# Kernel tuning notes

Hardware: AMD Instinct MI355X
Metric: run time of the kernel (lower is better)

Reference implementation:

```python
import jax, jax.numpy as jnp
import numpy as np

K_STEPS = 2  # number of staged propagation levels encoded in edge_mask


def _propagate(h, src, dst, mask, num_nodes):
    """KPropagate: K staged scatter-add steps over the edge list.

    Step k sums messages along edges with edge_mask == k; later steps
    propagate the freshly aggregated values (rule-node fan-out).
    """
    out = jnp.zeros_like(h)
    cur = h
    for k in range(K_STEPS):
        msg = jnp.where((mask == k)[:, None], cur[src], jnp.zeros((), h.dtype))  # [E, F]
        out = out + jax.ops.segment_sum(msg, dst, num_segments=num_nodes)
        cur = out
    return out


def setup_inputs() -> dict:
    key = jax.random.key(0)
    ks = jax.random.split(key, 8)
    V, R = 50000, 10000
    N = V + R
    E = 160000
    F_IN, F_OUT = 512, 128
    x = jax.random.normal(ks[0], (N, F_IN), dtype=jnp.float32)
    edge_index = jax.random.randint(ks[1], (2, E), 0, N, dtype=jnp.int64)
    edge_mask = jax.random.randint(ks[2], (E,), 0, K_STEPS, dtype=jnp.int64)
    # lin1: in_features -> in_features; lin2: in_features -> out_features
    s1 = 1.0 / np.sqrt(F_IN)
    W1 = jax.random.uniform(ks[3], (F_IN, F_IN), jnp.float32, -s1, s1)
    b1 = jax.random.uniform(ks[4], (F_IN,), jnp.float32, -s1, s1)
    W2 = jax.random.uniform(ks[5], (F_IN, F_OUT), jnp.float32, -s1, s1)
    b2 = jax.random.uniform(ks[6], (F_OUT,), jnp.float32, -s1, s1)
    return {"x": x, "edge_index": edge_index, "edge_mask": edge_mask,
            "vertex_cnt": V, "rule_cnt": R,
            "W1": W1, "b1": b1, "W2": W2, "b2": b2}


def reference(x, edge_index, edge_mask, vertex_cnt, rule_cnt, W1, b1, W2, b2):
    N = x.shape[0]  # == vertex_cnt + rule_cnt
    src, dst = edge_index[0], edge_index[1]
    h = x @ W1 + b1                                   # lin1
    h = jax.nn.relu(_propagate(h, src, dst, edge_mask, N))  # P1 -> relu
    h = h @ W2 + b2                                   # lin2
    h = _propagate(h, src, dst, edge_mask, N)         # P2
    # NOTE: original code computes log_softmax into `out` but returns x (=h).
    return h
```

## Files before the change

### kernel.cpp

```cpp
#include <hip/hip_runtime.h>

typedef __bf16 bf16x8 __attribute__((ext_vector_type(8)));
typedef float  floatx4 __attribute__((ext_vector_type(4)));
typedef unsigned short ushortx8 __attribute__((ext_vector_type(8)));
typedef unsigned short ushortx4 __attribute__((ext_vector_type(4)));
typedef unsigned short ushortx2 __attribute__((ext_vector_type(2)));

__device__ __forceinline__ float bf2f(unsigned short u) {
    return __uint_as_float(((unsigned)u) << 16);
}
__device__ __forceinline__ unsigned short f2bf(float f) {
    unsigned u = __float_as_uint(f);
    return (unsigned short)((u + 0x7FFFu + ((u >> 16) & 1u)) >> 16);
}

__device__ __forceinline__ void gload_lds16(const unsigned short* g, unsigned short* l) {
    __builtin_amdgcn_global_load_lds(
        (const __attribute__((address_space(1))) void*)g,
        (__attribute__((address_space(3))) void*)l, 16, 0, 0);
}

__global__ void cvt_f32_bf16_kernel(const float* __restrict__ in,
                                    unsigned short* __restrict__ out, int n4) {
    int i = blockIdx.x * blockDim.x + threadIdx.x;
    if (i >= n4) return;
    float4 v = ((const float4*)in)[i];
    ushortx4 o;
    o[0] = f2bf(v.x); o[1] = f2bf(v.y); o[2] = f2bf(v.z); o[3] = f2bf(v.w);
    ((ushortx4*)out)[i] = o;
}

__global__ void transpose_cvt_kernel(const float* __restrict__ in,
                                     unsigned short* __restrict__ out,
                                     int K, int N) {
    int idx = blockIdx.x * blockDim.x + threadIdx.x;
    if (idx >= K * N) return;
    int k = idx / N, n = idx - k * N;
    out[n * K + k] = f2bf(in[idx]);
}

__global__ void init_head_kernel(int* __restrict__ head, int n) {
    int i = blockIdx.x * blockDim.x + threadIdx.x;
    if (i < n) head[i] = -1;
}

__global__ void build_list_kernel(const int* __restrict__ ei, int E,
                                  int* __restrict__ head, int* __restrict__ nxt) {
    int e = blockIdx.x * blockDim.x + threadIdx.x;
    if (e >= E) return;
    int d = ei[E + e];
    nxt[e] = atomicExch(&head[d], e);
}

#define BM 128
#define BN 128
#define BK 32

__global__ __launch_bounds__(256) void gemm_bt_bias(
    const unsigned short* __restrict__ A,
    const unsigned short* __restrict__ Bt,
    const float* __restrict__ bias,
    unsigned short* __restrict__ C,
    int M, int N, int K)
{
    __shared__ unsigned short Sh[8192];
    unsigned short (*As)[512] = (unsigned short(*)[512])Sh;
    unsigned short (*Bs)[512] = (unsigned short(*)[512])(Sh + 4096);

    const int tid  = threadIdx.x;
    const int lane = tid & 63;
    const int wave = tid >> 6;
    const int bM = blockIdx.y * BM;
    const int bN = blockIdx.x * BN;
    const int wm = (wave >> 1) * 64;
    const int wn = (wave & 1) * 64;
    const int q    = lane >> 4;
    const int mrow = lane & 15;

    int rA0 = bM + wave * 16 + mrow;        if (rA0 >= M) rA0 = M - 1;
    int rA1 = bM + (wave + 4) * 16 + mrow;  if (rA1 >= M) rA1 = M - 1;
    const int rB0 = bN + wave * 16 + mrow;
    const int rB1 = bN + (wave + 4) * 16 + mrow;
    const unsigned short* gA0 = A  + (size_t)rA0 * K + q * 8;
    const unsigned short* gA1 = A  + (size_t)rA1 * K + q * 8;
    const unsigned short* gB0 = Bt + (size_t)rB0 * K + q * 8;
    const unsigned short* gB1 = Bt + (size_t)rB1 * K + q * 8;

    floatx4 acc[4][4];
#pragma unroll
    for (int i = 0; i < 4; i++)
#pragma unroll
        for (int j = 0; j < 4; j++) acc[i][j] = (floatx4)(0.0f);

    for (int kt = 0; kt < K; kt += BK) {
        gload_lds16(gA0 + kt, &As[wave][0]);
        gload_lds16(gA1 + kt, &As[wave + 4][0]);
        gload_lds16(gB0 + kt, &Bs[wave][0]);
        gload_lds16(gB1 + kt, &Bs[wave + 4][0]);
        __syncthreads();

        bf16x8 af[4], bfv[4];
#pragma unroll
        for (int mi = 0; mi < 4; mi++)
            af[mi] = *(const bf16x8*)&As[(wave >> 1) * 4 + mi][lane * 8];
#pragma unroll
        for (int ni = 0; ni < 4; ni++)
            bfv[ni] = *(const bf16x8*)&Bs[(wave & 1) * 4 + ni][lane * 8];
#pragma unroll
        for (int mi = 0; mi < 4; mi++)
#pragma unroll
            for (int ni = 0; ni < 4; ni++)
                acc[mi][ni] = __builtin_amdgcn_mfma_f32_16x16x32_bf16(
                    af[mi], bfv[ni], acc[mi][ni], 0, 0, 0);
        __syncthreads();
    }

    unsigned short* lbuf = Sh + wave * 2048;
    float bv[4];
#pragma unroll
    for (int ni = 0; ni < 4; ni++) bv[ni] = bias[bN + wn + ni * 16 + mrow];

#pragma unroll
    for (int p = 0; p < 2; p++) {
#pragma unroll
        for (int mh = 0; mh < 2; mh++) {
            int mi = 2 * p + mh;
#pragma unroll
            for (int ni = 0; ni < 4; ni++)
#pragma unroll
                for (int r = 0; r < 4; r++)
                    lbuf[(mh * 16 + q * 4 + r) * 64 + ni * 16 + mrow] =
                        f2bf(acc[mi][ni][r] + bv[ni]);
        }
#pragma unroll
        for (int i = 0; i < 4; i++) {
            int prow = i * 8 + (lane >> 3);
            int pcol = (lane & 7) * 8;
            int grow = bM + wm + p * 32 + prow;
            if (grow < M)
                *(ushortx8*)(C + (size_t)grow * N + bN + wn + pcol) =
                    *(const ushortx8*)&lbuf[prow * 64 + pcol];
        }
    }
}

template <int VEC> struct VecT;
template <> struct VecT<8> { typedef ushortx8 type; };
template <> struct VecT<2> { typedef ushortx2 type; };

template <int VEC, bool ADD_SELF, bool RELU, bool OUT_F32>
__global__ __launch_bounds__(256) void prop_step_kernel(
    const unsigned short* __restrict__ cur,
    void* __restrict__ outp,
    const int* __restrict__ head,
    const int* __restrict__ nxt,
    const int* __restrict__ esrc,
    const int* __restrict__ emask,
    int kval, int Nn)
{
    typedef typename VecT<VEC>::type VT;
    const int w = blockIdx.x * 4 + (threadIdx.x >> 6);
    if (w >= Nn) return;
    const int lane = threadIdx.x & 63;
    const int F = VEC * 64;
    const size_t off = (size_t)w * F + lane * VEC;

    float acc[VEC];
    if (ADD_SELF) {
        VT v = *(const VT*)(cur + off);
#pragma unroll
        for (int i = 0; i < VEC; i++) acc[i] = bf2f(v[i]);
    } else {
#pragma unroll
        for (int i = 0; i < VEC; i++) acc[i] = 0.0f;
    }

    for (int e = head[w]; e >= 0; e = nxt[e]) {
        if (emask[e] == kval) {
            int s = esrc[e];
            VT v = *(const VT*)(cur + (size_t)s * F + lane * VEC);
#pragma unroll
            for (int i = 0; i < VEC; i++) acc[i] += bf2f(v[i]);
        }
    }

#pragma unroll
    for (int i = 0; i < VEC; i++)
        if (RELU && acc[i] < 0.0f) acc[i] = 0.0f;

    if (OUT_F32) {
        float* out = (float*)outp;
        float2 o2;
#pragma unroll
        for (int i = 0; i < VEC; i += 2) {
            o2.x = acc[i]; o2.y = acc[i + 1];
            *(float2*)(out + off + i) = o2;
        }
    } else {
        VT o;
#pragma unroll
        for (int i = 0; i < VEC; i++) o[i] = f2bf(acc[i]);
        *(VT*)((unsigned short*)outp + off) = o;
    }
}

extern "C" void kernel_launch(void* const* d_in, const int* in_sizes, int n_in,
                              void* d_out, int out_size, void* d_ws, size_t ws_size,
                              hipStream_t stream)
{
    const float* x  = (const float*)d_in[0];
    const int*   ei = (const int*)d_in[1];
    const int*   em = (const int*)d_in[2];
    const float* W1 = (const float*)d_in[5];
    const float* b1 = (const float*)d_in[6];
    const float* W2 = (const float*)d_in[7];
    const float* b2 = (const float*)d_in[8];

    const int FIN = 512, FOUT = 128;
    const int Nn = in_sizes[0] / FIN;
    const int E  = in_sizes[2];

    char* ws = (char*)d_ws;
    size_t off = 0;
    auto alloc = [&](size_t bytes) -> char* {
        char* p = ws + off;
        off += (bytes + 255) & ~(size_t)255;
        return p;
    };
    unsigned short* W1t = (unsigned short*)alloc((size_t)FIN * FIN * 2);
    unsigned short* W2t = (unsigned short*)alloc((size_t)FIN * FOUT * 2);
    unsigned short* xb  = (unsigned short*)alloc((size_t)Nn * FIN * 2);
    unsigned short* h1  = (unsigned short*)alloc((size_t)Nn * FIN * 2);
    unsigned short* h2  = (unsigned short*)alloc((size_t)Nn * FOUT * 2);
    unsigned short* A2  = (unsigned short*)alloc((size_t)Nn * FOUT * 2);
    int* head = (int*)alloc((size_t)Nn * 4);
    int* nxt  = (int*)alloc((size_t)E * 4);
    unsigned short* A1 = xb;
    (void)ws_size; (void)n_in; (void)out_size;

    cvt_f32_bf16_kernel<<<((Nn * FIN / 4) + 255) / 256, 256, 0, stream>>>(x, xb, Nn * FIN / 4);
    transpose_cvt_kernel<<<(FIN * FIN + 255) / 256, 256, 0, stream>>>(W1, W1t, FIN, FIN);
    transpose_cvt_kernel<<<(FIN * FOUT + 255) / 256, 256, 0, stream>>>(W2, W2t, FIN, FOUT);

    init_head_kernel<<<(Nn + 255) / 256, 256, 0, stream>>>(head, Nn);
    build_list_kernel<<<(E + 255) / 256, 256, 0, stream>>>(ei, E, head, nxt);

    {
        dim3 grid(FIN / BN, (Nn + BM - 1) / BM);
        gemm_bt_bias<<<grid, 256, 0, stream>>>(xb, W1t, b1, h1, Nn, FIN, FIN);
    }

    {
        int grid = (Nn + 3) / 4;
        prop_step_kernel<8, false, false, false><<<grid, 256, 0, stream>>>(h1, A1, head, nxt, ei, em, 0, Nn);
        prop_step_kernel<8, true,  true,  false><<<grid, 256, 0, stream>>>(A1, h1, head, nxt, ei, em, 1, Nn);
    }

    {
        dim3 grid(FOUT / BN, (Nn + BM - 1) / BM);
        gemm_bt_bias<<<grid, 256, 0, stream>>>(h1, W2t, b2, h2, Nn, FOUT, FIN);
    }

    {
        int grid = (Nn + 3) / 4;
        prop_step_kernel<2, false, false, false><<<grid, 256, 0, stream>>>(h2, A2, head, nxt, ei, em, 0, Nn);
        prop_step_kernel<2, true,  false, true ><<<grid, 256, 0, stream>>>(A2, d_out, head, nxt, ei, em, 1, Nn);
    }
}
```

Before: 453.2 us.

## Split edge lists per mask step, double GEMM K-tile, swizzle block order

Edge linked lists are now built separately for each mask value, so every propagation step walks only its own edges and no longer reads or tests the mask per edge. The GEMM K-tile grows from 32 to 64, which doubles the LDS footprint and halves the number of barrier pairs. A block-index remap groups 8 row tiles per column tile when the grid is 4 wide, to improve L2 reuse of A. The cost is a head array twice as large and more LDS per block, which may lower occupancy.

Result: faster. 398.1 us (-12.2%).

```diff
diff --git a/kernel.cpp b/kernel.cpp
--- a/kernel.cpp
+++ b/kernel.cpp
@@ -44,17 +44,19 @@
     if (i < n) head[i] = -1;
 }
 
-__global__ void build_list_kernel(const int* __restrict__ ei, int E,
+__global__ void build_list_kernel(const int* __restrict__ ei, const int* __restrict__ em,
+                                  int E, int Nn,
                                   int* __restrict__ head, int* __restrict__ nxt) {
     int e = blockIdx.x * blockDim.x + threadIdx.x;
     if (e >= E) return;
     int d = ei[E + e];
-    nxt[e] = atomicExch(&head[d], e);
+    int m = em[e];
+    nxt[e] = atomicExch(&head[m * Nn + d], e);
 }
 
 #define BM 128
 #define BN 128
-#define BK 32
+#define BK 64
 
 __global__ __launch_bounds__(256) void gemm_bt_bias(
     const unsigned short* __restrict__ A,
@@ -63,28 +65,47 @@
     unsigned short* __restrict__ C,
     int M, int N, int K)
 {
-    __shared__ unsigned short Sh[8192];
+    __shared__ unsigned short Sh[16384];
     unsigned short (*As)[512] = (unsigned short(*)[512])Sh;
-    unsigned short (*Bs)[512] = (unsigned short(*)[512])(Sh + 4096);
+    unsigned short (*Bs)[512] = (unsigned short(*)[512])(Sh + 8192);
 
     const int tid  = threadIdx.x;
     const int lane = tid & 63;
     const int wave = tid >> 6;
-    const int bM = blockIdx.y * BM;
-    const int bN = blockIdx.x * BN;
+
+    int bx, by;
+    if (gridDim.x == 4) {
+        int id = blockIdx.y * 4 + blockIdx.x;
+        int full = (gridDim.y & ~7) * 4;
+        if (id < full) {
+            bx = (id >> 3) & 3;
+            by = (id >> 5) * 8 + (id & 7);
+        } else {
+            int t = id - full;
+            by = (gridDim.y & ~7) + (t >> 2);
+            bx = t & 3;
+        }
+    } else {
+        bx = blockIdx.x; by = blockIdx.y;
+    }
+    const int bM = by * BM;
+    const int bN = bx * BN;
     const int wm = (wave >> 1) * 64;
     const int wn = (wave & 1) * 64;
     const int q    = lane >> 4;
     const int mrow = lane & 15;
 
-    int rA0 = bM + wave * 16 + mrow;        if (rA0 >= M) rA0 = M - 1;
-    int rA1 = bM + (wave + 4) * 16 + mrow;  if (rA1 >= M) rA1 = M - 1;
-    const int rB0 = bN + wave * 16 + mrow;
-    const int rB1 = bN + (wave + 4) * 16 + mrow;
-    const unsigned short* gA0 = A  + (size_t)rA0 * K + q * 8;
-    const unsigned short* gA1 = A  + (size_t)rA1 * K + q * 8;
-    const unsigned short* gB0 = Bt + (size_t)rB0 * K + q * 8;
-    const unsigned short* gB1 = Bt + (size_t)rB1 * K + q * 8;
+    const unsigned short* pA[4];
+    const unsigned short* pB[4];
+#pragma unroll
+    for (int c = 0; c < 4; c++) {
+        int gg = wave + 4 * c;
+        int g7 = gg & 7, s = gg >> 3;
+        int rA = bM + g7 * 16 + mrow; if (rA >= M) rA = M - 1;
+        int rB = bN + g7 * 16 + mrow;
+        pA[c] = A  + (size_t)rA * K + s * 32 + q * 8;
+        pB[c] = Bt + (size_t)rB * K + s * 32 + q * 8;
+    }
 
     floatx4 acc[4][4];
 #pragma unroll
@@ -93,25 +114,29 @@
         for (int j = 0; j < 4; j++) acc[i][j] = (floatx4)(0.0f);
 
     for (int kt = 0; kt < K; kt += BK) {
-        gload_lds16(gA0 + kt, &As[wave][0]);
-        gload_lds16(gA1 + kt, &As[wave + 4][0]);
-        gload_lds16(gB0 + kt, &Bs[wave][0]);
-        gload_lds16(gB1 + kt, &Bs[wave + 4][0]);
+#pragma unroll
+        for (int c = 0; c < 4; c++) {
+            gload_lds16(pA[c] + kt, &As[wave + 4 * c][0]);
+            gload_lds16(pB[c] + kt, &Bs[wave + 4 * c][0]);
+        }
         __syncthreads();
 
-        bf16x8 af[4], bfv[4];
-#pragma unroll
-        for (int mi = 0; mi < 4; mi++)
-            af[mi] = *(const bf16x8*)&As[(wave >> 1) * 4 + mi][lane * 8];
-#pragma unroll
-        for (int ni = 0; ni < 4; ni++)
-            bfv[ni] = *(const bf16x8*)&Bs[(wave & 1) * 4 + ni][lane * 8];
-#pragma unroll
-        for (int mi = 0; mi < 4; mi++)
+#pragma unroll
+        for (int s = 0; s < 2; s++) {
+            bf16x8 af[4], bfv[4];
+#pragma unroll
+            for (int mi = 0; mi < 4; mi++)
+                af[mi] = *(const bf16x8*)&As[s * 8 + (wave >> 1) * 4 + mi][lane * 8];
 #pragma unroll
             for (int ni = 0; ni < 4; ni++)
-                acc[mi][ni] = __builtin_amdgcn_mfma_f32_16x16x32_bf16(
-                    af[mi], bfv[ni], acc[mi][ni], 0, 0, 0);
+                bfv[ni] = *(const bf16x8*)&Bs[s * 8 + (wave & 1) * 4 + ni][lane * 8];
+#pragma unroll
+            for (int mi = 0; mi < 4; mi++)
+#pragma unroll
+                for (int ni = 0; ni < 4; ni++)
+                    acc[mi][ni] = __builtin_amdgcn_mfma_f32_16x16x32_bf16(
+                        af[mi], bfv[ni], acc[mi][ni], 0, 0, 0);
+        }
         __syncthreads();
     }
 
@@ -155,8 +180,7 @@
     const int* __restrict__ head,
     const int* __restrict__ nxt,
     const int* __restrict__ esrc,
-    const int* __restrict__ emask,
-    int kval, int Nn)
+    int Nn)
 {
     typedef typename VecT<VEC>::type VT;
     const int w = blockIdx.x * 4 + (threadIdx.x >> 6);
@@ -176,12 +200,10 @@
     }
 
     for (int e = head[w]; e >= 0; e = nxt[e]) {
-        if (emask[e] == kval) {
-            int s = esrc[e];
-            VT v = *(const VT*)(cur + (size_t)s * F + lane * VEC);
-#pragma unroll
-            for (int i = 0; i < VEC; i++) acc[i] += bf2f(v[i]);
-        }
+        int s = esrc[e];
+        VT v = *(const VT*)(cur + (size_t)s * F + lane * VEC);
+#pragma unroll
+        for (int i = 0; i < VEC; i++) acc[i] += bf2f(v[i]);
     }
 
 #pragma unroll
@@ -233,7 +255,7 @@
     unsigned short* h1  = (unsigned short*)alloc((size_t)Nn * FIN * 2);
     unsigned short* h2  = (unsigned short*)alloc((size_t)Nn * FOUT * 2);
     unsigned short* A2  = (unsigned short*)alloc((size_t)Nn * FOUT * 2);
-    int* head = (int*)alloc((size_t)Nn * 4);
+    int* head = (int*)alloc((size_t)2 * Nn * 4);
     int* nxt  = (int*)alloc((size_t)E * 4);
     unsigned short* A1 = xb;
     (void)ws_size; (void)n_in; (void)out_size;
@@ -242,8 +264,8 @@
     transpose_cvt_kernel<<<(FIN * FIN + 255) / 256, 256, 0, stream>>>(W1, W1t, FIN, FIN);
     transpose_cvt_kernel<<<(FIN * FOUT + 255) / 256, 256, 0, stream>>>(W2, W2t, FIN, FOUT);
 
-    init_head_kernel<<<(Nn + 255) / 256, 256, 0, stream>>>(head, Nn);
-    build_list_kernel<<<(E + 255) / 256, 256, 0, stream>>>(ei, E, head, nxt);
+    init_head_kernel<<<(2 * Nn + 255) / 256, 256, 0, stream>>>(head, 2 * Nn);
+    build_list_kernel<<<(E + 255) / 256, 256, 0, stream>>>(ei, em, E, Nn, head, nxt);
 
     {
         dim3 grid(FIN / BN, (Nn + BM - 1) / BM);
@@ -252,8 +274,8 @@
 
     {
         int grid = (Nn + 3) / 4;
-        prop_step_kernel<8, false, false, false><<<grid, 256, 0, stream>>>(h1, A1, head, nxt, ei, em, 0, Nn);
-        prop_step_kernel<8, true,  true,  false><<<grid, 256, 0, stream>>>(A1, h1, head, nxt, ei, em, 1, Nn);
+        prop_step_kernel<8, false, false, false><<<grid, 256, 0, stream>>>(h1, A1, head,      nxt, ei, Nn);
+        prop_step_kernel<8, true,  true,  false><<<grid, 256, 0, stream>>>(A1, h1, head + Nn, nxt, ei, Nn);
     }
 
     {
@@ -263,7 +285,7 @@
 
     {
         int grid = (Nn + 3) / 4;
-        prop_step_kernel<2, false, false, false><<<grid, 256, 0, stream>>>(h2, A2, head, nxt, ei, em, 0, Nn);
-        prop_step_kernel<2, true,  false, true ><<<grid, 256, 0, stream>>>(A2, d_out, head, nxt, ei, em, 1, Nn);
-    }
-}
+        prop_step_kernel<2, false, false, false><<<grid, 256, 0, stream>>>(h2, A2, head,      nxt, ei, Nn);
+        prop_step_kernel<2, true,  false, true ><<<grid, 256, 0, stream>>>(A2, d_out, head + Nn, nxt, ei, Nn);
+    }
+}
```
